# Kernel optimization log

Measured on AMD Instinct MI355X. Metric: run time of the kernel, lower is better.

Reference implementation:

```python
import jax, jax.numpy as jnp
import numpy as np

OUT = 56          # roi_align / mask resolution
SCALE = 0.25      # spatial_scale (bases at stride 4)
CO = 14           # raw coefficient resolution


def _roi_align_one(feat, box):
    """torchvision roi_align, aligned=True, sampling_ratio=1.
    feat: [B, H, W] base maps for this roi's image; box: [4] = (x0,y0,x1,y1).
    Returns [B, OUT, OUT]."""
    H, W = feat.shape[1], feat.shape[2]
    s = box * SCALE - 0.5  # aligned=True half-pixel offset
    x0, y0, x1, y1 = s[0], s[1], s[2], s[3]
    bw = (x1 - x0) / OUT
    bh = (y1 - y0) / OUT
    # sampling_ratio=1 -> single sample at each bin center
    xs = x0 + (jnp.arange(OUT, dtype=feat.dtype) + 0.5) * bw
    ys = y0 + (jnp.arange(OUT, dtype=feat.dtype) + 0.5) * bh
    vy = (ys >= -1.0) & (ys <= H)
    vx = (xs >= -1.0) & (xs <= W)
    yc = jnp.clip(ys, 0.0, H - 1)
    xc = jnp.clip(xs, 0.0, W - 1)
    yl = jnp.clip(jnp.floor(yc).astype(jnp.int32), 0, H - 2); yh = yl + 1
    xl = jnp.clip(jnp.floor(xc).astype(jnp.int32), 0, W - 2); xh = xl + 1
    ly = yc - yl; hy = 1.0 - ly
    lx = xc - xl; hx = 1.0 - lx
    fll = feat[:, yl, :][:, :, xl]; flh = feat[:, yl, :][:, :, xh]
    fhl = feat[:, yh, :][:, :, xl]; fhh = feat[:, yh, :][:, :, xh]
    val = (hy[:, None] * (hx[None, :] * fll + lx[None, :] * flh)
           + ly[:, None] * (hx[None, :] * fhl + lx[None, :] * fhh))
    return val * (vy[:, None] & vx[None, :])


def _paste_masks(masks, boxes, img_h, img_w):
    """do_paste_mask: grid_sample(bilinear, align_corners=False, zero pad).
    The grid is separable (y depends on row, x on column), so express it as two
    batched matmuls with tent-kernel weights. masks: [N,56,56] -> [N,img_h,img_w]."""
    x0, y0, x1, y1 = (boxes[:, 0:1], boxes[:, 1:2], boxes[:, 2:3], boxes[:, 3:4])
    gy = ((jnp.arange(img_h, dtype=masks.dtype) + 0.5 - y0) / (y1 - y0)) * 2.0 - 1.0  # [N,H]
    gx = ((jnp.arange(img_w, dtype=masks.dtype) + 0.5 - x0) / (x1 - x0)) * 2.0 - 1.0  # [N,W]
    # unnormalize (align_corners=False): f = (g+1)*size/2 - 0.5
    fy = (gy + 1.0) * OUT * 0.5 - 0.5
    fx = (gx + 1.0) * OUT * 0.5 - 0.5
    idx = jnp.arange(OUT, dtype=masks.dtype)
    Wy = jnp.maximum(0.0, 1.0 - jnp.abs(fy[:, :, None] - idx))  # [N, img_h, 56]
    Wx = jnp.maximum(0.0, 1.0 - jnp.abs(fx[:, :, None] - idx))  # [N, img_w, 56]
    rows = jnp.einsum('nhm,nmw->nhw', Wy, masks)                # [N, img_h, 56]
    return jnp.einsum('nhw,nqw->nhq', rows, Wx)                 # [N, img_h, img_w]


def setup_inputs() -> dict:
    key = jax.random.key(0)
    ks = jax.random.split(key, 6)
    b_h, b_w = 136, 200                 # bases at stride 4 of a 544x800 image
    img_h, img_w = b_h * 4, b_w * 4
    N, Bb = 100, 4
    bases = jax.random.normal(ks[0], (1, Bb, b_h, b_w), jnp.float32)
    x0 = jax.random.uniform(ks[1], (N, 1), minval=0.0, maxval=img_w * 0.55)
    y0 = jax.random.uniform(ks[2], (N, 1), minval=0.0, maxval=img_h * 0.55)
    w = jax.random.uniform(ks[3], (N, 1), minval=32.0, maxval=img_w * 0.4)
    h = jax.random.uniform(ks[4], (N, 1), minval=32.0, maxval=img_h * 0.4)
    boxes = jnp.concatenate([x0, y0,
                             jnp.minimum(x0 + w, img_w - 1.0),
                             jnp.minimum(y0 + h, img_h - 1.0)], axis=1)
    top = jax.random.normal(ks[5], (N, Bb * CO * CO), jnp.float32)
    box_feat = jnp.concatenate([jnp.zeros((N, 1), jnp.float32), boxes, top], axis=1)
    return {"bases": bases, "box_feat": box_feat}


def reference(bases, box_feat):
    bidx = box_feat[:, 0].astype(jnp.int32)
    boxes = box_feat[:, 1:5]
    top_feat = box_feat[:, 5:]
    N = box_feat.shape[0]
    Bb, b_h, b_w = bases.shape[1], bases.shape[2], bases.shape[3]
    # roi_align over all detections
    rois = jax.vmap(lambda i, b: _roi_align_one(bases[i], b))(bidx, boxes)  # [N,B,56,56]
    # merge_bases: upsample 14->56 (bilinear, align_corners=False), softmax over bases, blend
    coeffs = top_feat.reshape(N, Bb, CO, CO)
    coeffs = jax.image.resize(coeffs, (N, Bb, OUT, OUT), method='bilinear')
    coeffs = jax.nn.softmax(coeffs, axis=1)
    masks = jax.nn.sigmoid(jnp.sum(rois * coeffs, axis=1))  # [N,56,56]
    return _paste_masks(masks, boxes, b_h * 4, b_w * 4)      # [N, 4*b_h, 4*b_w]
```

## Files before the change

### kernel.cpp

```cpp
#include <hip/hip_runtime.h>
#include <math.h>

#define OUTD 56
#define COD  14
#define BH   136
#define BW   200
#define IMGH 544
#define IMGW 800
#define BB   4
#define BFS  789


__device__ __forceinline__ float mask_value(
    const float* __restrict__ feat,
    const float* __restrict__ top,
    float sx0, float sy0, float bw, float bh,
    int y, int x) {
  const float ysv = sy0 + ((float)y + 0.5f) * bh;
  const float xsv = sx0 + ((float)x + 0.5f) * bw;
  const float valid =
      (ysv >= -1.0f && ysv <= (float)BH && xsv >= -1.0f && xsv <= (float)BW)
          ? 1.0f : 0.0f;
  const float yc = fminf(fmaxf(ysv, 0.0f), (float)(BH - 1));
  const float xc = fminf(fmaxf(xsv, 0.0f), (float)(BW - 1));
  int yl = (int)floorf(yc); yl = yl > (BH - 2) ? (BH - 2) : yl;
  int xl = (int)floorf(xc); xl = xl > (BW - 2) ? (BW - 2) : xl;
  const float ly = yc - (float)yl, hy = 1.0f - ly;
  const float lx = xc - (float)xl, hx = 1.0f - lx;
  const float w00 = hy * hx, w01 = hy * lx, w10 = ly * hx, w11 = ly * lx;

  float cyf = fminf(fmaxf(((float)y + 0.5f) * 0.25f - 0.5f, 0.0f), (float)(COD - 1));
  float cxf = fminf(fmaxf(((float)x + 0.5f) * 0.25f - 0.5f, 0.0f), (float)(COD - 1));
  int cyl = (int)floorf(cyf); cyl = cyl > (COD - 2) ? (COD - 2) : cyl;
  int cxl = (int)floorf(cxf); cxl = cxl > (COD - 2) ? (COD - 2) : cxl;
  const float cly = cyf - (float)cyl, chy = 1.0f - cly;
  const float clx = cxf - (float)cxl, chx = 1.0f - clx;
  const float cw00 = chy * chx, cw01 = chy * clx, cw10 = cly * chx, cw11 = cly * clx;

  float rvals[BB], cvals[BB];
#pragma unroll
  for (int b = 0; b < BB; ++b) {
    const float* fb = feat + b * BH * BW;
    const float r = w00 * fb[yl * BW + xl]       + w01 * fb[yl * BW + xl + 1] +
                    w10 * fb[(yl + 1) * BW + xl] + w11 * fb[(yl + 1) * BW + xl + 1];
    rvals[b] = r * valid;
    const float* tb = top + b * COD * COD;
    cvals[b] = cw00 * tb[cyl * COD + cxl]       + cw01 * tb[cyl * COD + cxl + 1] +
               cw10 * tb[(cyl + 1) * COD + cxl] + cw11 * tb[(cyl + 1) * COD + cxl + 1];
  }

  const float mx = fmaxf(fmaxf(cvals[0], cvals[1]), fmaxf(cvals[2], cvals[3]));
  float e[BB], s = 0.0f;
#pragma unroll
  for (int b = 0; b < BB; ++b) { e[b] = __expf(cvals[b] - mx); s += e[b]; }
  const float inv = 1.0f / s;
  float dot = 0.0f;
#pragma unroll
  for (int b = 0; b < BB; ++b) dot += rvals[b] * (e[b] * inv);
  return 1.0f / (1.0f + __expf(-dot));
}

__global__ __launch_bounds__(256) void fused_blend_paste(
    const float* __restrict__ bases,
    const float* __restrict__ box_feat,
    float4* __restrict__ out) {
  const int h = blockIdx.x;
  const int n = blockIdx.y;
  const int tid = threadIdx.x;

  const float* bf = box_feat + (size_t)n * BFS;
  const float x0 = bf[1], y0 = bf[2], x1 = bf[3], y1 = bf[4];

  float4* orow = out + ((size_t)n * IMGH + h) * (IMGW / 4);
  const float fy = ((float)h + 0.5f - y0) * ((float)OUTD / (y1 - y0)) - 0.5f;

  if (!(fy > -1.0f && fy < (float)OUTD)) {
    if (tid < IMGW / 4) orow[tid] = make_float4(0.f, 0.f, 0.f, 0.f);
    return;
  }

  const int ml = (int)floorf(fy);
  const float wy1 = fy - (float)ml;
  const float wy0 = 1.0f - wy1;

  __shared__ float mrow[2][OUTD];

  if (tid < 2 * OUTD) {
    const int r_idx = (tid >= OUTD) ? 1 : 0;
    const int x = tid - r_idx * OUTD;
    const int r = ml + r_idx;
    float val = 0.0f;
    if (r >= 0 && r < OUTD) {
      const int bidx = (int)bf[0];
      const float sx0 = x0 * 0.25f - 0.5f;
      const float sy0 = y0 * 0.25f - 0.5f;
      const float bwv = (x1 - x0) * 0.25f * (1.0f / OUTD);
      const float bhv = (y1 - y0) * 0.25f * (1.0f / OUTD);
      const float* feat = bases + (size_t)bidx * BB * BH * BW;
      val = mask_value(feat, bf + 5, sx0, sy0, bwv, bhv, r, x);
    }
    mrow[r_idx][x] = val;
  }
  __syncthreads();

  if (tid >= IMGW / 4) return;

  const float invw = (float)OUTD / (x1 - x0);
  float res[4];
#pragma unroll
  for (int i = 0; i < 4; ++i) {
    const int q = tid * 4 + i;
    const float fx = ((float)q + 0.5f - x0) * invw - 0.5f;
    float v = 0.0f;
    if (fx > -1.0f && fx < (float)OUTD) {
      const int xl = (int)floorf(fx);
      const float wx1 = fx - (float)xl;
      const float wx0 = 1.0f - wx1;
      const bool xlv = (xl >= 0);
      const bool xhv = (xl + 1 <= OUTD - 1);
      const int xls = xlv ? xl : 0;
      const int xhs = xhv ? (xl + 1) : 0;
      const float v00 = xlv ? mrow[0][xls] : 0.0f;
      const float v01 = xhv ? mrow[0][xhs] : 0.0f;
      const float v10 = xlv ? mrow[1][xls] : 0.0f;
      const float v11 = xhv ? mrow[1][xhs] : 0.0f;
      v = wy0 * (wx0 * v00 + wx1 * v01) + wy1 * (wx0 * v10 + wx1 * v11);
    }
    res[i] = v;
  }
  orow[tid] = make_float4(res[0], res[1], res[2], res[3]);
}

extern "C" void kernel_launch(void* const* d_in, const int* in_sizes, int n_in,
                              void* d_out, int out_size, void* d_ws, size_t ws_size,
                              hipStream_t stream) {
  const float* bases    = (const float*)d_in[0];
  const float* box_feat = (const float*)d_in[1];
  const int N = in_sizes[1] / BFS;

  dim3 grid(IMGH, N);
  fused_blend_paste<<<grid, 256, 0, stream>>>(bases, box_feat, (float4*)d_out);
}
```

Baseline: 198.2 us.

## Split fused kernel into mask computation and paste kernels to avoid recomputation

Computes the 56x56 blended mask once per detection in a separate kernel and stores it in workspace; the paste kernel then reads mask rows instead of recomputing roi_align, coefficient upsampling and softmax for every output row. This removes the repeated mask evaluation that each output row did for its two source rows. It also simplifies the horizontal interpolation with fma and clamped weights. The cost is an extra kernel launch and a global memory round trip for the masks.

```diff
diff --git a/kernel.cpp b/kernel.cpp
--- a/kernel.cpp
+++ b/kernel.cpp
@@ -10,14 +10,28 @@
 #define BB   4
 #define BFS  789
 
+__global__ __launch_bounds__(256) void mask_kernel(
+    const float* __restrict__ bases,
+    const float* __restrict__ box_feat,
+    float* __restrict__ masks) {
+  const int n = blockIdx.y;
+  const int p = blockIdx.x * 256 + threadIdx.x;
+  if (p >= OUTD * OUTD) return;
+  const int y = p / OUTD;
+  const int x = p - y * OUTD;
 
-__device__ __forceinline__ float mask_value(
-    const float* __restrict__ feat,
-    const float* __restrict__ top,
-    float sx0, float sy0, float bw, float bh,
-    int y, int x) {
-  const float ysv = sy0 + ((float)y + 0.5f) * bh;
-  const float xsv = sx0 + ((float)x + 0.5f) * bw;
+  const float* bf = box_feat + (size_t)n * BFS;
+  const int bidx = (int)bf[0];
+  const float x0 = bf[1], y0 = bf[2], x1 = bf[3], y1 = bf[4];
+  const float sx0 = x0 * 0.25f - 0.5f;
+  const float sy0 = y0 * 0.25f - 0.5f;
+  const float bwv = (x1 - x0) * 0.25f * (1.0f / OUTD);
+  const float bhv = (y1 - y0) * 0.25f * (1.0f / OUTD);
+  const float* feat = bases + (size_t)bidx * BB * BH * BW;
+  const float* top  = bf + 5;
+
+  const float ysv = sy0 + ((float)y + 0.5f) * bhv;
+  const float xsv = sx0 + ((float)x + 0.5f) * bwv;
   const float valid =
       (ysv >= -1.0f && ysv <= (float)BH && xsv >= -1.0f && xsv <= (float)BW)
           ? 1.0f : 0.0f;
@@ -57,11 +71,11 @@
   float dot = 0.0f;
 #pragma unroll
   for (int b = 0; b < BB; ++b) dot += rvals[b] * (e[b] * inv);
-  return 1.0f / (1.0f + __expf(-dot));
+  masks[(size_t)n * (OUTD * OUTD) + p] = 1.0f / (1.0f + __expf(-dot));
 }
 
-__global__ __launch_bounds__(256) void fused_blend_paste(
-    const float* __restrict__ bases,
+__global__ __launch_bounds__(256) void paste_kernel(
+    const float* __restrict__ masks,
     const float* __restrict__ box_feat,
     float4* __restrict__ out) {
   const int h = blockIdx.x;
@@ -69,9 +83,9 @@
   const int tid = threadIdx.x;
 
   const float* bf = box_feat + (size_t)n * BFS;
-  const float x0 = bf[1], y0 = bf[2], x1 = bf[3], y1 = bf[4];
+  const float y0 = bf[2], y1 = bf[4];
+  float4* orow = out + ((size_t)n * IMGH + h) * (IMGW / 4);
 
-  float4* orow = out + ((size_t)n * IMGH + h) * (IMGW / 4);
   const float fy = ((float)h + 0.5f - y0) * ((float)OUTD / (y1 - y0)) - 0.5f;
 
   if (!(fy > -1.0f && fy < (float)OUTD)) {
@@ -84,47 +98,39 @@
   const float wy0 = 1.0f - wy1;
 
   __shared__ float mrow[2][OUTD];
-
   if (tid < 2 * OUTD) {
     const int r_idx = (tid >= OUTD) ? 1 : 0;
     const int x = tid - r_idx * OUTD;
     const int r = ml + r_idx;
-    float val = 0.0f;
-    if (r >= 0 && r < OUTD) {
-      const int bidx = (int)bf[0];
-      const float sx0 = x0 * 0.25f - 0.5f;
-      const float sy0 = y0 * 0.25f - 0.5f;
-      const float bwv = (x1 - x0) * 0.25f * (1.0f / OUTD);
-      const float bhv = (y1 - y0) * 0.25f * (1.0f / OUTD);
-      const float* feat = bases + (size_t)bidx * BB * BH * BW;
-      val = mask_value(feat, bf + 5, sx0, sy0, bwv, bhv, r, x);
-    }
-    mrow[r_idx][x] = val;
+    float v = 0.0f;
+    if (r >= 0 && r < OUTD)
+      v = masks[(size_t)n * (OUTD * OUTD) + r * OUTD + x];
+    mrow[r_idx][x] = v;
   }
   __syncthreads();
 
   if (tid >= IMGW / 4) return;
 
+  const float x0 = bf[1], x1 = bf[3];
   const float invw = (float)OUTD / (x1 - x0);
+  const float cx = (0.5f - x0) * invw - 0.5f;
+
   float res[4];
 #pragma unroll
   for (int i = 0; i < 4; ++i) {
-    const int q = tid * 4 + i;
-    const float fx = ((float)q + 0.5f - x0) * invw - 0.5f;
+    const float q = (float)(tid * 4 + i);
+    const float fx = fmaf(q, invw, cx);
     float v = 0.0f;
     if (fx > -1.0f && fx < (float)OUTD) {
       const int xl = (int)floorf(fx);
-      const float wx1 = fx - (float)xl;
-      const float wx0 = 1.0f - wx1;
-      const bool xlv = (xl >= 0);
-      const bool xhv = (xl + 1 <= OUTD - 1);
-      const int xls = xlv ? xl : 0;
-      const int xhs = xhv ? (xl + 1) : 0;
-      const float v00 = xlv ? mrow[0][xls] : 0.0f;
-      const float v01 = xhv ? mrow[0][xhs] : 0.0f;
-      const float v10 = xlv ? mrow[1][xls] : 0.0f;
-      const float v11 = xhv ? mrow[1][xhs] : 0.0f;
-      v = wy0 * (wx0 * v00 + wx1 * v01) + wy1 * (wx0 * v10 + wx1 * v11);
+      float wx1 = fx - (float)xl;
+      float wx0 = 1.0f - wx1;
+      const int xls = xl < 0 ? 0 : xl;
+      const int xhs = (xl + 1 > OUTD - 1) ? (OUTD - 1) : (xl + 1);
+      if (xl < 0) wx0 = 0.0f;
+      if (xl + 1 > OUTD - 1) wx1 = 0.0f;
+      v = wy0 * (wx0 * mrow[0][xls] + wx1 * mrow[0][xhs]) +
+          wy1 * (wx0 * mrow[1][xls] + wx1 * mrow[1][xhs]);
     }
     res[i] = v;
   }
@@ -138,6 +144,11 @@
   const float* box_feat = (const float*)d_in[1];
   const int N = in_sizes[1] / BFS;
 
-  dim3 grid(IMGH, N);
-  fused_blend_paste<<<grid, 256, 0, stream>>>(bases, box_feat, (float4*)d_out);
+  float* masks = (float*)d_ws;
+
+  dim3 g1((OUTD * OUTD + 255) / 256, N);
+  mask_kernel<<<g1, 256, 0, stream>>>(bases, box_feat, masks);
+
+  dim3 g2(IMGH, N);
+  paste_kernel<<<g2, 256, 0, stream>>>(masks, box_feat, (float4*)d_out);
 }
```

After: 175.0 us. 1.13x faster.
